# Optimization experiments

Measured on AMD Instinct MI355X. Metric: run time of the kernel, lower is better.

## Reference

```python
import jax, jax.numpy as jnp
import numpy as np

T, D, H, B = 2048, 1152, 16, 8
DH = D // H  # 72


def _apply_rope(x, cos_h, sin_h):
    # x: [T, H, DH]; cos_h, sin_h: [T, DH//2] (already chunked halves)
    c = jnp.concatenate([cos_h, cos_h], axis=-1)[:, None, :]  # [T,1,DH]
    s = jnp.concatenate([sin_h, sin_h], axis=-1)[:, None, :]
    x1, x2 = jnp.split(x, 2, axis=-1)
    rot = jnp.concatenate([-x2, x1], axis=-1)
    return x * c + rot * s


def setup_inputs() -> dict:
    key = jax.random.key(0)
    ks = jax.random.split(key, 12)
    hidden_states = jax.random.normal(ks[0], (T, D), jnp.float32)
    inner = jnp.sort(jax.random.randint(ks[1], (B - 1,), 1, T))
    cu_seqlens = jnp.concatenate(
        [jnp.zeros((1,), jnp.int32), inner.astype(jnp.int32), jnp.full((1,), T, jnp.int32)])
    cos = jax.random.uniform(ks[2], (T, DH), jnp.float32, -1.0, 1.0)
    sin = jax.random.uniform(ks[3], (T, DH), jnp.float32, -1.0, 1.0)
    std = 0.02
    Wq = jax.random.normal(ks[4], (D, D), jnp.float32) * std
    Wk = jax.random.normal(ks[5], (D, D), jnp.float32) * std
    Wv = jax.random.normal(ks[6], (D, D), jnp.float32) * std
    Wo = jax.random.normal(ks[7], (D, D), jnp.float32) * std
    bq = jnp.zeros((D,), jnp.float32)
    bk = jnp.zeros((D,), jnp.float32)
    bv = jnp.zeros((D,), jnp.float32)
    bo = jnp.zeros((D,), jnp.float32)
    return {"hidden_states": hidden_states, "cu_seqlens": cu_seqlens,
            "cos": cos, "sin": sin,
            "Wq": Wq, "bq": bq, "Wk": Wk, "bk": bk,
            "Wv": Wv, "bv": bv, "Wo": Wo, "bo": bo}


def reference(hidden_states, cu_seqlens, cos, sin, Wq, bq, Wk, bk, Wv, bv, Wo, bo):
    t = hidden_states.shape[0]
    scale = DH ** -0.5
    q = (hidden_states @ Wq.T + bq).reshape(t, H, DH)
    k = (hidden_states @ Wk.T + bk).reshape(t, H, DH)
    v = (hidden_states @ Wv.T + bv).reshape(t, H, DH)
    # RoPE: cos/sin [T, DH] are chunked in half along last dim, first half used
    cos_h = cos[:, : DH // 2]
    sin_h = sin[:, : DH // 2]
    q = _apply_rope(q, cos_h, sin_h)
    k = _apply_rope(k, cos_h, sin_h)
    # segment ids from cu_seqlens -> block-diagonal (varlen) attention mask
    pos = jnp.arange(t)
    seg = jnp.searchsorted(cu_seqlens, pos, side='right') - 1  # [T]
    mask = seg[:, None] == seg[None, :]  # [T, T]
    scores = jnp.einsum('thd,shd->hts', q, k) * scale  # [H, T, T]
    scores = jnp.where(mask[None], scores, jnp.float32(-1e30))
    attn = jax.nn.softmax(scores, axis=-1)
    out = jnp.einsum('hts,shd->thd', attn, v).reshape(t, D)
    return out @ Wo.T + bo
```

## Files before the change

### kernel.cpp

```cpp
#include <hip/hip_runtime.h>

#define TT 2048
#define DM 1152
#define NHEAD 16
#define HDIM 72
#define HDP 96
#define HDV 80
#define KSPLIT 2

typedef __attribute__((ext_vector_type(8))) __bf16 bf16x8;
typedef __attribute__((ext_vector_type(4))) float f32x4;
typedef unsigned short u16;
typedef unsigned int u32;

__device__ inline u16 f2bf(float f){
  u32 u = __builtin_bit_cast(u32, f);
  return (u16)((u + 0x7FFFu + ((u >> 16) & 1u)) >> 16);
}
__device__ inline float bf2f(u16 v){
  return __builtin_bit_cast(float, ((u32)v) << 16);
}
__device__ inline bf16x8 ldb8(const u16* p){
  uint4 u = *(const uint4*)p;
  return __builtin_bit_cast(bf16x8, u);
}
__device__ inline f32x4 mfma16(bf16x8 a, bf16x8 b, f32x4 c){
  return __builtin_amdgcn_mfma_f32_16x16x32_bf16(a, b, c, 0, 0, 0);
}
__device__ inline void gload_lds16(const u16* g, u16* l){
  __builtin_amdgcn_global_load_lds(
      (const __attribute__((address_space(1))) void*)g,
      (__attribute__((address_space(3))) void*)l, 16, 0, 0);
}

__global__ void k_convert(const float* hid, const float* wq, const float* wk,
                          const float* wv, const float* wo, const int* cu,
                          u16* hb, u16* wqb, u16* wkb, u16* wvb, u16* wob,
                          u16* qhb, u16* khb, int* seg)
{
  long i = (long)blockIdx.x * blockDim.x + threadIdx.x;
  const long NHID = (long)TT * DM;
  const long NW = (long)DM * DM;
  const long NCV = NHID + 4*NW;
  if (i < NHID) {
    hb[i] = f2bf(hid[i]);
  } else if (i < NCV) {
    long j = i - NHID;
    int w = (int)(j / NW);
    long o = j - (long)w * NW;
    const float* src = (w==0)?wq:(w==1)?wk:(w==2)?wv:wo;
    u16* dst = (w==0)?wqb:(w==1)?wkb:(w==2)?wvb:wob;
    dst[o] = f2bf(src[o]);
  } else {
    long j = i - NCV;
    const long PER = (long)NHEAD*TT*12;
    int arr = (int)(j / PER);
    long r = j - (long)arr*PER;
    long th = r / 12;
    int c = (int)(r - th*12);
    ((u32*)(arr ? khb : qhb))[th*48 + 36 + c] = 0u;
  }
  if (i < TT) {
    int c = 0;
    for (int e = 0; e < 9; ++e) c += (cu[e] <= (int)i);
    seg[i] = c - 1;
  }
}

__device__ __forceinline__ void gemm128_body(const u16* __restrict__ A,
                                             const u16* __restrict__ W,
                                             const float* __restrict__ bias,
                                             void* out, int mode, float oscale)
{
  __shared__ __align__(16) u16 As[128*32];
  __shared__ __align__(16) u16 Bs[128*32];
  int tid = threadIdx.x;
  int lane = tid & 63, wid = tid >> 6;
  int l15 = lane & 15, quad = lane >> 4;
  int bm = blockIdx.x * 128, bn = blockIdx.y * 128;
  int wm = (wid>>1)*64, wn = (wid&1)*64;
  f32x4 acc[4][4] = {};
  const u16* ga = A + (long)(bm + (tid>>2))*DM + (tid&3)*8;
  const u16* gb = W + (long)(bn + (tid>>2))*DM + (tid&3)*8;
  u16* lA = As + wid*512;
  u16* lB = Bs + wid*512;
  for (int k0 = 0; k0 < DM; k0 += 32) {
    gload_lds16(ga + k0,          lA);
    gload_lds16(ga + k0 + 64*DM,  lA + 2048);
    gload_lds16(gb + k0,          lB);
    gload_lds16(gb + k0 + 64*DM,  lB + 2048);
    __syncthreads();
    bf16x8 af[4], bfr[4];
    for (int i=0;i<4;i++) af[i]  = ldb8(As + (wm + i*16 + l15)*32 + quad*8);
    for (int i=0;i<4;i++) bfr[i] = ldb8(Bs + (wn + i*16 + l15)*32 + quad*8);
    for (int mi=0;mi<4;mi++)
      for (int ni=0;ni<4;ni++)
        acc[mi][ni] = mfma16(af[mi], bfr[ni], acc[mi][ni]);
    __syncthreads();
  }
  for (int ni=0;ni<4;ni++){
    int n = bn + wn + ni*16 + l15;
    float bv_ = bias[n];
    int h = n / HDIM, dh = n - (n / HDIM)*HDIM;
    for (int mi=0;mi<4;mi++){
      int m0 = bm + wm + mi*16 + quad*4;
      for (int r=0;r<4;r++){
        float v = (acc[mi][ni][r] + bv_) * oscale;
        int m = m0 + r;
        if (mode == 0) {
          ((u16*)out)[((long)(h*TT + m))*HDP + dh] = f2bf(v);
        } else {
          ((u16*)out)[((long)(h*HDV + dh))*TT + m] = f2bf(v);
        }
      }
    }
  }
}

__global__ __launch_bounds__(256) void k_gemm_qkv(const u16* __restrict__ A,
    const u16* __restrict__ Wq, const u16* __restrict__ Wk, const u16* __restrict__ Wv,
    const float* __restrict__ bq, const float* __restrict__ bk, const float* __restrict__ bv,
    u16* oq, u16* ok, u16* ov)
{
  const float scale = 0.11785113019775793f;
  int z = blockIdx.z;
  if (z == 0)      gemm128_body(A, Wq, bq, oq, 0, scale);
  else if (z == 1) gemm128_body(A, Wk, bk, ok, 0, 1.0f);
  else             gemm128_body(A, Wv, bv, ov, 2, 1.0f);
}

__global__ __launch_bounds__(256) void k_gemm_o(const u16* __restrict__ A,
    const u16* __restrict__ W, const float* __restrict__ bias, float* out)
{
  __shared__ __align__(16) u16 As[64*32];
  __shared__ __align__(16) u16 Bs[128*32];
  int tid = threadIdx.x;
  int lane = tid & 63, wid = tid >> 6;
  int l15 = lane & 15, quad = lane >> 4;
  int bm = blockIdx.x * 64, bn = blockIdx.y * 128;
  int wm = (wid>>1)*32, wn = (wid&1)*64;
  f32x4 acc[2][4] = {};
  const u16* ga = A + (long)(bm + (tid>>2))*DM + (tid&3)*8;
  const u16* gb = W + (long)(bn + (tid>>2))*DM + (tid&3)*8;
  u16* lA = As + wid*512;
  u16* lB = Bs + wid*512;
  for (int k0 = 0; k0 < DM; k0 += 32) {
    gload_lds16(ga + k0,          lA);
    gload_lds16(gb + k0,          lB);
    gload_lds16(gb + k0 + 64*DM,  lB + 2048);
    __syncthreads();
    bf16x8 af[2], bfr[4];
    for (int i=0;i<2;i++) af[i]  = ldb8(As + (wm + i*16 + l15)*32 + quad*8);
    for (int i=0;i<4;i++) bfr[i] = ldb8(Bs + (wn + i*16 + l15)*32 + quad*8);
    for (int mi=0;mi<2;mi++)
      for (int ni=0;ni<4;ni++)
        acc[mi][ni] = mfma16(af[mi], bfr[ni], acc[mi][ni]);
    __syncthreads();
  }
  for (int ni=0;ni<4;ni++){
    int n = bn + wn + ni*16 + l15;
    float bv_ = bias[n];
    for (int mi=0;mi<2;mi++){
      int m0 = bm + wm + mi*16 + quad*4;
      for (int r=0;r<4;r++)
        out[(long)(m0 + r)*DM + n] = acc[mi][ni][r] + bv_;
    }
  }
}

__global__ void k_rope(u16* qh, u16* kh, const float* __restrict__ cosb,
                       const float* __restrict__ sinb)
{
  int i = blockIdx.x * blockDim.x + threadIdx.x;
  const int total = 2 * NHEAD * TT * 36;
  if (i >= total) return;
  int d = i % 36; int rest = i / 36;
  int t = rest % TT; rest /= TT;
  int h = rest % NHEAD; int qk = rest / NHEAD;
  u16* base = (qk ? kh : qh) + ((long)h*TT + t)*HDP;
  float x1 = bf2f(base[d]), x2 = bf2f(base[d+36]);
  float c = cosb[t*HDIM + d], s = sinb[t*HDIM + d];
  base[d]    = f2bf(x1*c - x2*s);
  base[d+36] = f2bf(x2*c + x1*s);
}

__global__ __launch_bounds__(256) void k_attn(const u16* __restrict__ qh,
                                              const u16* __restrict__ kh,
                                              const u16* __restrict__ vT,
                                              const int* __restrict__ seg,
                                              const int* __restrict__ cu,
                                              float* __restrict__ pacc,
                                              float* __restrict__ plsum)
{
  __shared__ __align__(16) u16 Ks[2][64*96];
  __shared__ __align__(16) u16 pbuf[4][16][72];
  int h = blockIdx.y;
  int z = blockIdx.z;
  int tid = threadIdx.x, lane = tid & 63, wid = tid >> 6;
  int l15 = lane & 15, quad = lane >> 4;
  int qb0 = blockIdx.x * 64;
  int qbase = qb0 + wid*16;

  const u16* qp = qh + ((long)h*TT + qbase + l15)*HDP + quad*8;
  bf16x8 qf0 = ldb8(qp), qf1 = ldb8(qp+32), qf2 = ldb8(qp+64);
  int segq[4];
  for (int r=0;r<4;r++) segq[r] = seg[qbase + quad*4 + r];
  f32x4 acc[5] = {};
  float lsum[4] = {0.f, 0.f, 0.f, 0.f};

  int seg_lo = seg[qb0], seg_hi = seg[qb0 + 63];
  int s_begin = cu[seg_lo] & ~63;
  int s_end = cu[seg_hi + 1];
  int nt = (s_end - s_begin + 63) >> 6;
  int nt0 = (nt + 1) >> 1;
  int it_lo = z ? nt0 : 0;
  int it_hi = z ? nt : nt0;

  const u16* kbase = kh + (long)h*TT*HDP;

  if (it_lo < it_hi) {
    {
      const u16* gk = kbase + (long)(s_begin + it_lo*64)*HDP + tid*8;
      u16* lK = Ks[0] + wid*512;
      gload_lds16(gk,        lK);
      gload_lds16(gk + 2048, lK + 2048);
      gload_lds16(gk + 4096, lK + 4096);
    }
    for (int it = it_lo; it < it_hi; ++it) {
      int s0 = s_begin + it*64;
      int cur = (it - it_lo) & 1;
      __syncthreads();
      if (it + 1 < it_hi) {
        const u16* gk = kbase + (long)(s0 + 64)*HDP + tid*8;
        u16* lK = Ks[cur^1] + wid*512;
        gload_lds16(gk,        lK);
        gload_lds16(gk + 2048, lK + 2048);
        gload_lds16(gk + 4096, lK + 4096);
      }
      f32x4 sc[4] = {};
      for (int j=0;j<4;j++){
        const u16* kp = Ks[cur] + (j*16 + l15)*96 + quad*8;
        sc[j] = mfma16(qf0, ldb8(kp),    sc[j]);
        sc[j] = mfma16(qf1, ldb8(kp+32), sc[j]);
        sc[j] = mfma16(qf2, ldb8(kp+64), sc[j]);
      }
      int sg[4];
      for (int j=0;j<4;j++) sg[j] = seg[s0 + j*16 + l15];
      float p[4][4];
      for (int j=0;j<4;j++)
        for (int r=0;r<4;r++){
          p[j][r] = (sg[j] == segq[r]) ? __expf(sc[j][r]) : 0.f;
          lsum[r] += p[j][r];
        }
      for (int j=0;j<4;j++)
        for (int r=0;r<4;r++)
          pbuf[wid][quad*4+r][j*16+l15] = f2bf(p[j][r]);
      bf16x8 pf0 = ldb8(&pbuf[wid][l15][quad*8]);
      bf16x8 pf1 = ldb8(&pbuf[wid][l15][32 + quad*8]);
      const u16* vp = vT + ((long)h*HDV + l15)*TT + s0 + quad*8;
      for (int n=0;n<5;n++){
        bf16x8 vf0 = ldb8(vp + (long)n*16*TT);
        bf16x8 vf1 = ldb8(vp + (long)n*16*TT + 32);
        acc[n] = mfma16(pf0, vf0, acc[n]);
        acc[n] = mfma16(pf1, vf1, acc[n]);
      }
    }
  }
  for (int off=1; off<16; off<<=1)
    for (int r=0;r<4;r++)
      lsum[r] += __shfl_xor(lsum[r], off, 64);
  for (int n=0;n<5;n++){
    int dh = n*16 + l15;
    for (int r=0;r<4;r++){
      int t = qbase + quad*4 + r;
      pacc[(((long)z*TT + t)*NHEAD + h)*HDV + dh] = acc[n][r];
    }
  }
  if (l15 == 0){
    for (int r=0;r<4;r++){
      int t = qbase + quad*4 + r;
      plsum[((long)z*TT + t)*NHEAD + h] = lsum[r];
    }
  }
}

__global__ void k_combine(const float* __restrict__ pacc,
                          const float* __restrict__ plsum,
                          u16* __restrict__ ao)
{
  int i = blockIdx.x*blockDim.x + threadIdx.x;
  const int total = TT*NHEAD*HDIM;
  if (i >= total) return;
  int dh = i % HDIM; int rest = i / HDIM;
  int h = rest % NHEAD; int t = rest / NHEAD;
  long i0 = ((long)t*NHEAD + h)*HDV + dh;
  float a = pacc[i0] + pacc[(long)TT*NHEAD*HDV + i0];
  float l = plsum[t*NHEAD + h] + plsum[TT*NHEAD + t*NHEAD + h];
  ao[(long)t*DM + h*HDIM + dh] = f2bf(a / l);
}

extern "C" void kernel_launch(void* const* d_in, const int* in_sizes, int n_in,
                              void* d_out, int out_size, void* d_ws, size_t ws_size,
                              hipStream_t stream)
{
  const float* hid  = (const float*)d_in[0];
  const int*   cu   = (const int*)d_in[1];
  const float* cosb = (const float*)d_in[2];
  const float* sinb = (const float*)d_in[3];
  const float* wq   = (const float*)d_in[4];
  const float* bq   = (const float*)d_in[5];
  const float* wk   = (const float*)d_in[6];
  const float* bk   = (const float*)d_in[7];
  const float* wv   = (const float*)d_in[8];
  const float* bv   = (const float*)d_in[9];
  const float* wo   = (const float*)d_in[10];
  const float* bo   = (const float*)d_in[11];

  char* ws = (char*)d_ws;
  u16* hb  = (u16*)ws; ws += (long)TT*DM*2;
  u16* wqb = (u16*)ws; ws += (long)DM*DM*2;
  u16* wkb = (u16*)ws; ws += (long)DM*DM*2;
  u16* wvb = (u16*)ws; ws += (long)DM*DM*2;
  u16* wob = (u16*)ws; ws += (long)DM*DM*2;
  u16* qhb = (u16*)ws; ws += (long)NHEAD*TT*HDP*2;
  u16* khb = (u16*)ws; ws += (long)NHEAD*TT*HDP*2;
  u16* vTb = (u16*)ws; ws += (long)NHEAD*HDV*TT*2;
  u16* aob = (u16*)ws; ws += (long)TT*DM*2;
  int* seg = (int*)ws; ws += (long)TT*4;
  float* pacc  = (float*)ws; ws += (long)KSPLIT*TT*NHEAD*HDV*4;
  float* plsum = (float*)ws; ws += (long)KSPLIT*TT*NHEAD*4;

  long nconv = (long)TT*DM + 4L*DM*DM + 2L*NHEAD*TT*12;
  k_convert<<<dim3((nconv + 255)/256), 256, 0, stream>>>(
      hid, wq, wk, wv, wo, cu, hb, wqb, wkb, wvb, wob, qhb, khb, seg);

  dim3 gqkv(TT/128, DM/128, 3);
  k_gemm_qkv<<<gqkv, 256, 0, stream>>>(hb, wqb, wkb, wvb, bq, bk, bv, qhb, khb, vTb);

  int nrope = 2*NHEAD*TT*36;
  k_rope<<<dim3((nrope + 255)/256), 256, 0, stream>>>(qhb, khb, cosb, sinb);

  dim3 ga(TT/64, NHEAD, KSPLIT);
  k_attn<<<ga, 256, 0, stream>>>(qhb, khb, vTb, seg, cu, pacc, plsum);

  int ncomb = TT*NHEAD*HDIM;
  k_combine<<<dim3((ncomb + 255)/256), 256, 0, stream>>>(pacc, plsum, aob);

  dim3 go(TT/64, DM/128);
  k_gemm_o<<<go, 256, 0, stream>>>(aob, wob, bo, (float*)d_out);
}
```

Before: 205.4 us.

## Load K tiles directly from global memory and mask by segment bounds

Removes the double-buffered shared-memory staging of K tiles and the per-iteration block barrier, so each wave loads its K fragments straight from global memory into registers. The per-key segment-id gathers are replaced by comparing key indices against precomputed cu_seqlens bounds for each query row. Launch bounds now request 4 blocks per CU to raise occupancy. This trades LDS reuse across the four waves for independent global/L2 loads and no barrier, and may add register pressure and global traffic.

```diff
diff --git a/kernel.cpp b/kernel.cpp
--- a/kernel.cpp
+++ b/kernel.cpp
@@ -184,15 +184,14 @@
   base[d+36] = f2bf(x2*c + x1*s);
 }
 
-__global__ __launch_bounds__(256) void k_attn(const u16* __restrict__ qh,
-                                              const u16* __restrict__ kh,
-                                              const u16* __restrict__ vT,
-                                              const int* __restrict__ seg,
-                                              const int* __restrict__ cu,
-                                              float* __restrict__ pacc,
-                                              float* __restrict__ plsum)
-{
-  __shared__ __align__(16) u16 Ks[2][64*96];
+__global__ __launch_bounds__(256, 4) void k_attn(const u16* __restrict__ qh,
+                                                 const u16* __restrict__ kh,
+                                                 const u16* __restrict__ vT,
+                                                 const int* __restrict__ seg,
+                                                 const int* __restrict__ cu,
+                                                 float* __restrict__ pacc,
+                                                 float* __restrict__ plsum)
+{
   __shared__ __align__(16) u16 pbuf[4][16][72];
   int h = blockIdx.y;
   int z = blockIdx.z;
@@ -203,67 +202,57 @@
 
   const u16* qp = qh + ((long)h*TT + qbase + l15)*HDP + quad*8;
   bf16x8 qf0 = ldb8(qp), qf1 = ldb8(qp+32), qf2 = ldb8(qp+64);
-  int segq[4];
-  for (int r=0;r<4;r++) segq[r] = seg[qbase + quad*4 + r];
+  int lo[4], hi[4];
+  for (int r=0;r<4;r++){
+    int sq = seg[qbase + quad*4 + r];
+    lo[r] = cu[sq]; hi[r] = cu[sq+1];
+  }
   f32x4 acc[5] = {};
   float lsum[4] = {0.f, 0.f, 0.f, 0.f};
 
-  int seg_lo = seg[qb0], seg_hi = seg[qb0 + 63];
-  int s_begin = cu[seg_lo] & ~63;
-  int s_end = cu[seg_hi + 1];
+  int s_begin = cu[seg[qb0]] & ~63;
+  int s_end = cu[seg[qb0 + 63] + 1];
   int nt = (s_end - s_begin + 63) >> 6;
   int nt0 = (nt + 1) >> 1;
   int it_lo = z ? nt0 : 0;
   int it_hi = z ? nt : nt0;
 
   const u16* kbase = kh + (long)h*TT*HDP;
-
-  if (it_lo < it_hi) {
-    {
-      const u16* gk = kbase + (long)(s_begin + it_lo*64)*HDP + tid*8;
-      u16* lK = Ks[0] + wid*512;
-      gload_lds16(gk,        lK);
-      gload_lds16(gk + 2048, lK + 2048);
-      gload_lds16(gk + 4096, lK + 4096);
-    }
-    for (int it = it_lo; it < it_hi; ++it) {
-      int s0 = s_begin + it*64;
-      int cur = (it - it_lo) & 1;
-      __syncthreads();
-      if (it + 1 < it_hi) {
-        const u16* gk = kbase + (long)(s0 + 64)*HDP + tid*8;
-        u16* lK = Ks[cur^1] + wid*512;
-        gload_lds16(gk,        lK);
-        gload_lds16(gk + 2048, lK + 2048);
-        gload_lds16(gk + 4096, lK + 4096);
+  const u16* vbase = vT + ((long)h*HDV + l15)*TT + quad*8;
+
+  for (int it = it_lo; it < it_hi; ++it) {
+    int s0 = s_begin + it*64;
+    const u16* kp = kbase + (long)(s0 + l15)*HDP + quad*8;
+    bf16x8 kf[4][3];
+    for (int j=0;j<4;j++)
+      for (int c=0;c<3;c++)
+        kf[j][c] = ldb8(kp + j*16*HDP + c*32);
+    f32x4 sc[4] = {};
+    for (int j=0;j<4;j++){
+      sc[j] = mfma16(qf0, kf[j][0], sc[j]);
+      sc[j] = mfma16(qf1, kf[j][1], sc[j]);
+      sc[j] = mfma16(qf2, kf[j][2], sc[j]);
+    }
+    float p[4][4];
+    for (int j=0;j<4;j++){
+      int kidx = s0 + j*16 + l15;
+      for (int r=0;r<4;r++){
+        bool in = (kidx >= lo[r]) && (kidx < hi[r]);
+        p[j][r] = in ? __expf(sc[j][r]) : 0.f;
+        lsum[r] += p[j][r];
       }
-      f32x4 sc[4] = {};
-      for (int j=0;j<4;j++){
-        const u16* kp = Ks[cur] + (j*16 + l15)*96 + quad*8;
-        sc[j] = mfma16(qf0, ldb8(kp),    sc[j]);
-        sc[j] = mfma16(qf1, ldb8(kp+32), sc[j]);
-        sc[j] = mfma16(qf2, ldb8(kp+64), sc[j]);
-      }
-      int sg[4];
-      for (int j=0;j<4;j++) sg[j] = seg[s0 + j*16 + l15];
-      float p[4][4];
-      for (int j=0;j<4;j++)
-        for (int r=0;r<4;r++){
-          p[j][r] = (sg[j] == segq[r]) ? __expf(sc[j][r]) : 0.f;
-          lsum[r] += p[j][r];
-        }
-      for (int j=0;j<4;j++)
-        for (int r=0;r<4;r++)
-          pbuf[wid][quad*4+r][j*16+l15] = f2bf(p[j][r]);
-      bf16x8 pf0 = ldb8(&pbuf[wid][l15][quad*8]);
-      bf16x8 pf1 = ldb8(&pbuf[wid][l15][32 + quad*8]);
-      const u16* vp = vT + ((long)h*HDV + l15)*TT + s0 + quad*8;
-      for (int n=0;n<5;n++){
-        bf16x8 vf0 = ldb8(vp + (long)n*16*TT);
-        bf16x8 vf1 = ldb8(vp + (long)n*16*TT + 32);
-        acc[n] = mfma16(pf0, vf0, acc[n]);
-        acc[n] = mfma16(pf1, vf1, acc[n]);
-      }
+    }
+    for (int j=0;j<4;j++)
+      for (int r=0;r<4;r++)
+        pbuf[wid][quad*4+r][j*16+l15] = f2bf(p[j][r]);
+    bf16x8 pf0 = ldb8(&pbuf[wid][l15][quad*8]);
+    bf16x8 pf1 = ldb8(&pbuf[wid][l15][32 + quad*8]);
+    const u16* vp = vbase + s0;
+    for (int n=0;n<5;n++){
+      bf16x8 vf0 = ldb8(vp + (long)n*16*TT);
+      bf16x8 vf1 = ldb8(vp + (long)n*16*TT + 32);
+      acc[n] = mfma16(pf0, vf0, acc[n]);
+      acc[n] = mfma16(pf1, vf1, acc[n]);
     }
   }
   for (int off=1; off<16; off<<=1)
```

Result: slower. 216.1 us (+5.2%).
